# Kernel optimization log

Hardware: AMD Instinct MI355X
Metric: run time of the kernel (lower is better)

The kernel has to match this reference:

```python
import jax, jax.numpy as jnp
import numpy as np

N_NODES = 100000
N_EDGES = 1600000
NEG_SLOPE = 0.2


def gat_conv(x, W, al, ar, src, dst, n_nodes):
    """DGL-style GATConv. x:[N,Fin] W:[Fin,H*D] al,ar:[H,D] -> [N,H,D]."""
    H, D = al.shape
    h = (x @ W).reshape(-1, H, D)                      # [N,H,D]
    el = jnp.sum(h * al, axis=-1)                      # [N,H]
    er = jnp.sum(h * ar, axis=-1)                      # [N,H]
    e = jax.nn.leaky_relu(el[src] + er[dst], NEG_SLOPE)  # [E,H]
    # segment softmax over edges grouped by destination node
    m = jax.ops.segment_max(e, dst, num_segments=n_nodes)  # [N,H]
    ex = jnp.exp(e - m[dst])                           # [E,H]
    s = jax.ops.segment_sum(ex, dst, num_segments=n_nodes)  # [N,H]
    alpha = ex / s[dst]                                # [E,H]
    msg = h[src] * alpha[..., None]                    # [E,H,D]
    return jax.ops.segment_sum(msg, dst, num_segments=n_nodes)  # [N,H,D]


def setup_inputs() -> dict:
    key = jax.random.key(0)
    ks = jax.random.split(key, 9)
    in_dim, hid, out_dim, heads = 128, 32, 64, 4
    x = jax.random.normal(ks[0], (N_NODES, in_dim), dtype=jnp.float32)
    src = jax.random.randint(ks[1], (N_EDGES,), 0, N_NODES, dtype=jnp.int32)
    dst = jax.random.randint(ks[2], (N_EDGES,), 0, N_NODES, dtype=jnp.int32)
    sc1 = 1.0 / np.sqrt(in_dim)
    sc2 = 1.0 / np.sqrt(heads * hid)
    W1 = jax.random.normal(ks[3], (in_dim, heads * hid), dtype=jnp.float32) * sc1
    al1 = jax.random.normal(ks[4], (heads, hid), dtype=jnp.float32) * sc1
    ar1 = jax.random.normal(ks[5], (heads, hid), dtype=jnp.float32) * sc1
    W2 = jax.random.normal(ks[6], (heads * hid, out_dim), dtype=jnp.float32) * sc2
    al2 = jax.random.normal(ks[7], (1, out_dim), dtype=jnp.float32) * sc2
    ar2 = jax.random.normal(ks[8], (1, out_dim), dtype=jnp.float32) * sc2
    return {"x": x, "src": src, "dst": dst, "W1": W1, "al1": al1, "ar1": ar1,
            "W2": W2, "al2": al2, "ar2": ar2}


def reference(x, src, dst, W1, al1, ar1, W2, al2, ar2):
    h = gat_conv(x, W1, al1, ar1, src, dst, N_NODES)   # [N,4,32]
    h = h.reshape(h.shape[0], -1)                      # flatten(1) -> [N,128]
    h = jax.nn.selu(h)                                 # dropout is identity in eval
    out = gat_conv(h, W2, al2, ar2, src, dst, N_NODES) # [N,1,64]
    return out.mean(axis=1)                            # [N,64]
```

## Files before the change

kernel.cpp:

```cpp
#include <hip/hip_runtime.h>
#include <hip/hip_fp16.h>

#define N_NODES 100000
#define N_EDGES 1600000
#define NP1 (N_NODES + 1)
#define NB 391
#define CHUNK 6250
#define NBLK 256
#define BPAD 4736

typedef _Float16 half8 __attribute__((ext_vector_type(8)));
typedef float f32x4 __attribute__((ext_vector_type(4)));

static __device__ __forceinline__ unsigned pkh2(float a, float b) {
    __half2 t = __floats2half2_rn(a, b);
    return *(unsigned*)&t;
}

__global__ __launch_bounds__(256) void k_gemm1(
    const float* __restrict__ x, const float* __restrict__ W,
    const float* __restrict__ al, const float* __restrict__ ar,
    __half* __restrict__ h, float* __restrict__ el, float* __restrict__ er)
{
    __shared__ _Float16 Wt[128 * 136];
    __shared__ _Float16 xs[64 * 136];
    const int tid = threadIdx.x;
    const int n0 = blockIdx.x * 64;

    #pragma unroll
    for (int pass = 0; pass < 16; ++pass) {
        int k  = (tid >> 5) + pass * 8;
        int c4 = (tid & 31) * 4;
        float4 w = *(const float4*)(W + (size_t)k * 128 + c4);
        Wt[(c4 + 0) * 136 + k] = (_Float16)w.x;
        Wt[(c4 + 1) * 136 + k] = (_Float16)w.y;
        Wt[(c4 + 2) * 136 + k] = (_Float16)w.z;
        Wt[(c4 + 3) * 136 + k] = (_Float16)w.w;
    }
    {
        int row = tid >> 2, kq = (tid & 3) * 32;
        int n = n0 + row;
        _Float16* d = xs + row * 136 + kq;
        if (n < N_NODES) {
            const float* xp = x + (size_t)n * 128 + kq;
            #pragma unroll
            for (int j = 0; j < 8; ++j) {
                float4 v = *(const float4*)(xp + j * 4);
                d[j*4+0] = (_Float16)v.x; d[j*4+1] = (_Float16)v.y;
                d[j*4+2] = (_Float16)v.z; d[j*4+3] = (_Float16)v.w;
            }
        } else {
            #pragma unroll
            for (int j = 0; j < 32; ++j) d[j] = (_Float16)0.f;
        }
    }
    __syncthreads();

    const int wv = tid >> 6, l = tid & 63;
    const int r0 = wv * 16;
    const int lc = l & 15, lk = l >> 4;

    half8 afr[4];
    #pragma unroll
    for (int ks = 0; ks < 4; ++ks)
        afr[ks] = *(const half8*)(xs + (r0 + lc) * 136 + ks * 32 + lk * 8);
    __syncthreads();

    float eh_l[4][4], eh_r[4][4];
    #pragma unroll
    for (int hd = 0; hd < 4; ++hd)
        #pragma unroll
        for (int i = 0; i < 4; ++i) { eh_l[hd][i] = 0.f; eh_r[hd][i] = 0.f; }

    f32x4 accs[8];
    #pragma unroll
    for (int ct = 0; ct < 8; ++ct) {
        f32x4 acc = {0.f, 0.f, 0.f, 0.f};
        #pragma unroll
        for (int ks = 0; ks < 4; ++ks) {
            half8 b = *(const half8*)(Wt + (ct * 16 + lc) * 136 + ks * 32 + lk * 8);
            acc = __builtin_amdgcn_mfma_f32_16x16x32_f16(afr[ks], b, acc, 0, 0, 0);
        }
        accs[ct] = acc;
        float a_l = al[ct * 16 + lc], a_r = ar[ct * 16 + lc];
        #pragma unroll
        for (int i = 0; i < 4; ++i) {
            eh_l[ct >> 1][i] = fmaf(acc[i], a_l, eh_l[ct >> 1][i]);
            eh_r[ct >> 1][i] = fmaf(acc[i], a_r, eh_r[ct >> 1][i]);
        }
    }

    #pragma unroll
    for (int ct = 0; ct < 8; ++ct)
        #pragma unroll
        for (int i = 0; i < 4; ++i)
            xs[(r0 + lk * 4 + i) * 136 + ct * 16 + lc] = (_Float16)accs[ct][i];

    #pragma unroll
    for (int hd = 0; hd < 4; ++hd)
        #pragma unroll
        for (int i = 0; i < 4; ++i) {
            float v = eh_l[hd][i];
            v += __shfl_xor(v, 1); v += __shfl_xor(v, 2);
            v += __shfl_xor(v, 4); v += __shfl_xor(v, 8);
            eh_l[hd][i] = v;
            float u = eh_r[hd][i];
            u += __shfl_xor(u, 1); u += __shfl_xor(u, 2);
            u += __shfl_xor(u, 4); u += __shfl_xor(u, 8);
            eh_r[hd][i] = u;
        }
    if (lc == 0) {
        #pragma unroll
        for (int i = 0; i < 4; ++i) {
            int n = n0 + r0 + lk * 4 + i;
            if (n < N_NODES) {
                #pragma unroll
                for (int hd = 0; hd < 4; ++hd) {
                    el[n * 4 + hd] = eh_l[hd][i];
                    er[n * 4 + hd] = eh_r[hd][i];
                }
            }
        }
    }
    __syncthreads();
    {
        int row = tid >> 2, kq = (tid & 3) * 32;
        int n = n0 + row;
        if (n < N_NODES) {
            #pragma unroll
            for (int j = 0; j < 4; ++j)
                *(uint4*)(h + (size_t)n * 128 + kq + j * 8) =
                    *(const uint4*)(xs + row * 136 + kq + j * 8);
        }
    }
}

__global__ __launch_bounds__(256) void k_gemm2(
    const __half* __restrict__ in, const float* __restrict__ W,
    const float* __restrict__ al, const float* __restrict__ ar,
    __half* __restrict__ h, float* __restrict__ el, float* __restrict__ er)
{
    __shared__ _Float16 Wt[64 * 136];
    __shared__ _Float16 xs[64 * 136];
    const int tid = threadIdx.x;
    const int n0 = blockIdx.x * 64;
    const float SC = 1.0507009873554805f;
    const float AL = 1.6732632423543772f;

    #pragma unroll
    for (int pass = 0; pass < 8; ++pass) {
        int k  = (tid >> 4) + pass * 16;
        int c4 = (tid & 15) * 4;
        float4 w = *(const float4*)(W + (size_t)k * 64 + c4);
        Wt[(c4 + 0) * 136 + k] = (_Float16)w.x;
        Wt[(c4 + 1) * 136 + k] = (_Float16)w.y;
        Wt[(c4 + 2) * 136 + k] = (_Float16)w.z;
        Wt[(c4 + 3) * 136 + k] = (_Float16)w.w;
    }
    {
        int row = tid >> 2, kq = (tid & 3) * 32;
        int n = n0 + row;
        _Float16* d = xs + row * 136 + kq;
        if (n < N_NODES) {
            const __half* ip = in + (size_t)n * 128 + kq;
            #pragma unroll
            for (int j = 0; j < 8; ++j) {
                uint2 u = *(const uint2*)(ip + j * 4);
                float2 f01 = __half22float2(*(__half2*)&u.x);
                float2 f23 = __half22float2(*(__half2*)&u.y);
                float v0 = f01.x > 0.f ? SC * f01.x : SC * AL * (__expf(f01.x) - 1.f);
                float v1 = f01.y > 0.f ? SC * f01.y : SC * AL * (__expf(f01.y) - 1.f);
                float v2 = f23.x > 0.f ? SC * f23.x : SC * AL * (__expf(f23.x) - 1.f);
                float v3 = f23.y > 0.f ? SC * f23.y : SC * AL * (__expf(f23.y) - 1.f);
                d[j*4+0] = (_Float16)v0; d[j*4+1] = (_Float16)v1;
                d[j*4+2] = (_Float16)v2; d[j*4+3] = (_Float16)v3;
            }
        } else {
            #pragma unroll
            for (int j = 0; j < 32; ++j) d[j] = (_Float16)0.f;
        }
    }
    __syncthreads();

    const int wv = tid >> 6, l = tid & 63;
    const int r0 = wv * 16;
    const int lc = l & 15, lk = l >> 4;

    half8 afr[4];
    #pragma unroll
    for (int ks = 0; ks < 4; ++ks)
        afr[ks] = *(const half8*)(xs + (r0 + lc) * 136 + ks * 32 + lk * 8);
    __syncthreads();

    float pl[4], pr[4];
    #pragma unroll
    for (int i = 0; i < 4; ++i) { pl[i] = 0.f; pr[i] = 0.f; }

    f32x4 accs[4];
    #pragma unroll
    for (int ct = 0; ct < 4; ++ct) {
        f32x4 acc = {0.f, 0.f, 0.f, 0.f};
        #pragma unroll
        for (int ks = 0; ks < 4; ++ks) {
            half8 b = *(const half8*)(Wt + (ct * 16 + lc) * 136 + ks * 32 + lk * 8);
            acc = __builtin_amdgcn_mfma_f32_16x16x32_f16(afr[ks], b, acc, 0, 0, 0);
        }
        accs[ct] = acc;
        float a_l = al[ct * 16 + lc], a_r = ar[ct * 16 + lc];
        #pragma unroll
        for (int i = 0; i < 4; ++i) {
            pl[i] = fmaf(acc[i], a_l, pl[i]);
            pr[i] = fmaf(acc[i], a_r, pr[i]);
        }
    }

    #pragma unroll
    for (int ct = 0; ct < 4; ++ct)
        #pragma unroll
        for (int i = 0; i < 4; ++i)
            xs[(r0 + lk * 4 + i) * 136 + ct * 16 + lc] = (_Float16)accs[ct][i];

    #pragma unroll
    for (int i = 0; i < 4; ++i) {
        float v = pl[i];
        v += __shfl_xor(v, 1); v += __shfl_xor(v, 2);
        v += __shfl_xor(v, 4); v += __shfl_xor(v, 8);
        pl[i] = v;
        float u = pr[i];
        u += __shfl_xor(u, 1); u += __shfl_xor(u, 2);
        u += __shfl_xor(u, 4); u += __shfl_xor(u, 8);
        pr[i] = u;
    }
    if (lc == 0) {
        #pragma unroll
        for (int i = 0; i < 4; ++i) {
            int n = n0 + r0 + lk * 4 + i;
            if (n < N_NODES) { el[n] = pl[i]; er[n] = pr[i]; }
        }
    }
    __syncthreads();
    {
        int row = tid >> 2, kq = (tid & 3) * 16;
        int n = n0 + row;
        if (n < N_NODES) {
            #pragma unroll
            for (int j = 0; j < 2; ++j)
                *(uint4*)(h + (size_t)n * 64 + kq + j * 8) =
                    *(const uint4*)(xs + row * 136 + kq + j * 8);
        }
    }
}

__global__ __launch_bounds__(256) void k_place(
    const int* __restrict__ src, const int* __restrict__ dst,
    int* __restrict__ cursor, unsigned* __restrict__ pairs)
{
    __shared__ int cnt[NB], basev[NB];
    const int tid = threadIdx.x;
    for (int j = tid; j < NB; j += 256) cnt[j] = 0;
    __syncthreads();
    int beg = blockIdx.x * CHUNK, end = beg + CHUNK;
    for (int i = beg + tid; i < end; i += 256)
        atomicAdd(&cnt[dst[i] >> 8], 1);
    __syncthreads();
    for (int j = tid; j < NB; j += 256)
        basev[j] = cnt[j] ? atomicAdd(&cursor[j], cnt[j]) : 0;
    __syncthreads();
    for (int j = tid; j < NB; j += 256) cnt[j] = 0;
    __syncthreads();
    for (int i = beg + tid; i < end; i += 256) {
        int d = dst[i];
        int b = d >> 8;
        int r = atomicAdd(&cnt[b], 1);
        pairs[(size_t)b * BPAD + basev[b] + r] =
            ((unsigned)(d & 255) << 17) | (unsigned)src[i];
    }
}

__global__ __launch_bounds__(256) void k_csr(
    const unsigned* __restrict__ pairs, const int* __restrict__ cursor,
    unsigned* __restrict__ rowdeg, int* __restrict__ csr_src)
{
    __shared__ int cnt[256], exc[256];
    const int b = blockIdx.x;
    const int tid = threadIdx.x;
    cnt[tid] = 0;
    __syncthreads();
    int beg = b * BPAD;
    int end = beg + cursor[b];
    for (int i = beg + tid; i < end; i += 256)
        atomicAdd(&cnt[pairs[i] >> 17], 1);
    __syncthreads();
    int v = cnt[tid];
    exc[tid] = v;
    __syncthreads();
    for (int o = 1; o < 256; o <<= 1) {
        int t = (tid >= o) ? exc[tid - o] : 0;
        __syncthreads();
        exc[tid] += t;
        __syncthreads();
    }
    int excl = exc[tid] - v;
    int node = b * 256 + tid;
    if (node < N_NODES)
        rowdeg[node] = ((unsigned)(beg + excl) << 8) | (unsigned)v;
    __syncthreads();
    exc[tid] = beg + excl;
    cnt[tid] = 0;
    __syncthreads();
    for (int i = beg + tid; i < end; i += 256) {
        unsigned e = pairs[i];
        int dl = (int)(e >> 17);
        int r = atomicAdd(&cnt[dl], 1);
        csr_src[exc[dl] + r] = (int)(e & 0x1FFFFu);
    }
}

__global__ __launch_bounds__(256) void k_fused1(
    const unsigned* __restrict__ rowdeg, const int* __restrict__ csr_src,
    const __half* __restrict__ h,
    const float* __restrict__ el,
    const float* __restrict__ er,
    __half* __restrict__ out)
{
    __shared__ int    s_sx[4][64];
    __shared__ __half s_p[4][64][4];
    const int w = threadIdx.x >> 6;
    int node = (blockIdx.x << 2) + w;
    int lane = threadIdx.x & 63;
    if (node >= N_NODES) return;
    unsigned rd = rowdeg[node];
    int rs = (int)(rd >> 8), deg = (int)(rd & 255u);
    int re = rs + deg;
    const int q = lane & 15, g = lane >> 4;
    const int hq = q >> 2;
    float4 erd = ((const float4*)er)[node];
    float m0, m1, m2, m3;
    float s0 = 0.f, s1 = 0.f, s2 = 0.f, s3 = 0.f;
    __half2 acc2[4];
    #pragma unroll
    for (int k = 0; k < 4; ++k) acc2[k] = __half2half2((__half)0.f);

    auto agg = [&](int nch) {
        int nit4 = (nch + 15) >> 4;
        for (int t = 0; t < nit4; ++t) {
            int eb = t * 16 + g;
            int sj0 = s_sx[w][eb];
            int sj1 = s_sx[w][eb + 4];
            int sj2 = s_sx[w][eb + 8];
            int sj3 = s_sx[w][eb + 12];
            __half2 a0 = __half2half2(s_p[w][eb][hq]);
            __half2 a1 = __half2half2(s_p[w][eb + 4][hq]);
            __half2 a2 = __half2half2(s_p[w][eb + 8][hq]);
            __half2 a3 = __half2half2(s_p[w][eb + 12][hq]);
            uint4 v0 = *((const uint4*)(h + (size_t)sj0 * 128) + q);
            uint4 v1 = *((const uint4*)(h + (size_t)sj1 * 128) + q);
            uint4 v2 = *((const uint4*)(h + (size_t)sj2 * 128) + q);
            uint4 v3 = *((const uint4*)(h + (size_t)sj3 * 128) + q);
            acc2[0] = __hfma2(*(__half2*)&v0.x, a0, acc2[0]);
            acc2[1] = __hfma2(*(__half2*)&v0.y, a0, acc2[1]);
            acc2[2] = __hfma2(*(__half2*)&v0.z, a0, acc2[2]);
            acc2[3] = __hfma2(*(__half2*)&v0.w, a0, acc2[3]);
            acc2[0] = __hfma2(*(__half2*)&v1.x, a1, acc2[0]);
            acc2[1] = __hfma2(*(__half2*)&v1.y, a1, acc2[1]);
            acc2[2] = __hfma2(*(__half2*)&v1.z, a1, acc2[2]);
            acc2[3] = __hfma2(*(__half2*)&v1.w, a1, acc2[3]);
            acc2[0] = __hfma2(*(__half2*)&v2.x, a2, acc2[0]);
            acc2[1] = __hfma2(*(__half2*)&v2.y, a2, acc2[1]);
            acc2[2] = __hfma2(*(__half2*)&v2.z, a2, acc2[2]);
            acc2[3] = __hfma2(*(__half2*)&v2.w, a2, acc2[3]);
            acc2[0] = __hfma2(*(__half2*)&v3.x, a3, acc2[0]);
            acc2[1] = __hfma2(*(__half2*)&v3.y, a3, acc2[1]);
            acc2[2] = __hfma2(*(__half2*)&v3.z, a3, acc2[2]);
            acc2[3] = __hfma2(*(__half2*)&v3.w, a3, acc2[3]);
        }
    };

    if (re > rs) {
        int nch = min(64, re - rs);
        int sidx = 0;
        float e0 = -INFINITY, e1 = -INFINITY, e2 = -INFINITY, e3 = -INFINITY;
        if (lane < nch) {
            sidx = csr_src[rs + lane];
            float4 l4 = ((const float4*)el)[sidx];
            e0 = l4.x + erd.x; e0 = e0 >= 0.f ? e0 : 0.2f * e0;
            e1 = l4.y + erd.y; e1 = e1 >= 0.f ? e1 : 0.2f * e1;
            e2 = l4.z + erd.z; e2 = e2 >= 0.f ? e2 : 0.2f * e2;
            e3 = l4.w + erd.w; e3 = e3 >= 0.f ? e3 : 0.2f * e3;
        }
        float c0 = e0, c1 = e1, c2 = e2, c3 = e3;
        #pragma unroll
        for (int o = 32; o > 0; o >>= 1) {
            c0 = fmaxf(c0, __shfl_xor(c0, o));
            c1 = fmaxf(c1, __shfl_xor(c1, o));
            c2 = fmaxf(c2, __shfl_xor(c2, o));
            c3 = fmaxf(c3, __shfl_xor(c3, o));
        }
        m0 = c0; m1 = c1; m2 = c2; m3 = c3;
        float p0 = __expf(e0 - m0), p1 = __expf(e1 - m1);
        float p2 = __expf(e2 - m2), p3 = __expf(e3 - m3);
        s_sx[w][lane] = sidx;
        *(__half2*)&s_p[w][lane][0] = __floats2half2_rn(p0, p1);
        *(__half2*)&s_p[w][lane][2] = __floats2half2_rn(p2, p3);
        float q0 = p0, q1 = p1, q2 = p2, q3 = p3;
        #pragma unroll
        for (int o = 32; o > 0; o >>= 1) {
            q0 += __shfl_xor(q0, o);
            q1 += __shfl_xor(q1, o);
            q2 += __shfl_xor(q2, o);
            q3 += __shfl_xor(q3, o);
        }
        s0 = q0; s1 = q1; s2 = q2; s3 = q3;
        agg(nch);

        for (int base = rs + 64; base < re; base += 64) {
            nch = min(64, re - base);
            sidx = 0;
            e0 = e1 = e2 = e3 = -INFINITY;
            if (lane < nch) {
                sidx = csr_src[base + lane];
                float4 l4 = ((const float4*)el)[sidx];
                e0 = l4.x + erd.x; e0 = e0 >= 0.f ? e0 : 0.2f * e0;
                e1 = l4.y + erd.y; e1 = e1 >= 0.f ? e1 : 0.2f * e1;
                e2 = l4.z + erd.z; e2 = e2 >= 0.f ? e2 : 0.2f * e2;
                e3 = l4.w + erd.w; e3 = e3 >= 0.f ? e3 : 0.2f * e3;
            }
            c0 = e0; c1 = e1; c2 = e2; c3 = e3;
            #pragma unroll
            for (int o = 32; o > 0; o >>= 1) {
                c0 = fmaxf(c0, __shfl_xor(c0, o));
                c1 = fmaxf(c1, __shfl_xor(c1, o));
                c2 = fmaxf(c2, __shfl_xor(c2, o));
                c3 = fmaxf(c3, __shfl_xor(c3, o));
            }
            float n0 = fmaxf(m0, c0), n1 = fmaxf(m1, c1);
            float n2 = fmaxf(m2, c2), n3 = fmaxf(m3, c3);
            float r0 = __expf(m0 - n0), r1 = __expf(m1 - n1);
            float r2 = __expf(m2 - n2), r3 = __expf(m3 - n3);
            p0 = __expf(e0 - n0); p1 = __expf(e1 - n1);
            p2 = __expf(e2 - n2); p3 = __expf(e3 - n3);
            s_sx[w][lane] = sidx;
            *(__half2*)&s_p[w][lane][0] = __floats2half2_rn(p0, p1);
            *(__half2*)&s_p[w][lane][2] = __floats2half2_rn(p2, p3);
            q0 = p0; q1 = p1; q2 = p2; q3 = p3;
            #pragma unroll
            for (int o = 32; o > 0; o >>= 1) {
                q0 += __shfl_xor(q0, o);
                q1 += __shfl_xor(q1, o);
                q2 += __shfl_xor(q2, o);
                q3 += __shfl_xor(q3, o);
            }
            s0 = s0 * r0 + q0; s1 = s1 * r1 + q1;
            s2 = s2 * r2 + q2; s3 = s3 * r3 + q3;
            float rh = hq == 0 ? r0 : hq == 1 ? r1 : hq == 2 ? r2 : r3;
            __half2 rh2 = __half2half2((__half)rh);
            #pragma unroll
            for (int k = 0; k < 4; ++k) acc2[k] = __hmul2(acc2[k], rh2);
            m0 = n0; m1 = n1; m2 = n2; m3 = n3;
            agg(nch);
        }
    }

    float sh = hq == 0 ? s0 : hq == 1 ? s1 : hq == 2 ? s2 : s3;
    float inv = (re > rs) ? 1.f / sh : 0.f;
    float acc[8];
    #pragma unroll
    for (int k = 0; k < 4; ++k) {
        float2 f = __half22float2(acc2[k]);
        acc[2*k] = f.x * inv; acc[2*k+1] = f.y * inv;
    }
    #pragma unroll
    for (int k = 0; k < 8; ++k) {
        acc[k] += __shfl_xor(acc[k], 16);
        acc[k] += __shfl_xor(acc[k], 32);
    }
    if (g == 0) {
        uint4 o;
        o.x = pkh2(acc[0], acc[1]);
        o.y = pkh2(acc[2], acc[3]);
        o.z = pkh2(acc[4], acc[5]);
        o.w = pkh2(acc[6], acc[7]);
        *((uint4*)(out + (size_t)node * 128) + q) = o;
    }
}

__global__ __launch_bounds__(256) void k_fused2(
    const unsigned* __restrict__ rowdeg, const int* __restrict__ csr_src,
    const __half* __restrict__ h,
    const float* __restrict__ el,
    const float* __restrict__ er,
    float* __restrict__ out)
{
    __shared__ int    s_sx[4][64];
    __shared__ __half s_p[4][64];
    const int w = threadIdx.x >> 6;
    int node = (blockIdx.x << 2) + w;
    int lane = threadIdx.x & 63;
    if (node >= N_NODES) return;
    unsigned rd = rowdeg[node];
    int rs = (int)(rd >> 8), deg = (int)(rd & 255u);
    int re = rs + deg;
    const int q = lane & 7, g = lane >> 3;
    float erd = er[node];
    float m, s = 0.f;
    __half2 acc2[4];
    #pragma unroll
    for (int k = 0; k < 4; ++k) acc2[k] = __half2half2((__half)0.f);

    auto agg = [&](int nch) {
        int nit4 = (nch + 31) >> 5;
        for (int t = 0; t < nit4; ++t) {
            int eb = t * 32 + g;
            int sj0 = s_sx[w][eb];
            int sj1 = s_sx[w][eb + 8];
            int sj2 = s_sx[w][eb + 16];
            int sj3 = s_sx[w][eb + 24];
            __half2 a0 = __half2half2(s_p[w][eb]);
            __half2 a1 = __half2half2(s_p[w][eb + 8]);
            __half2 a2 = __half2half2(s_p[w][eb + 16]);
            __half2 a3 = __half2half2(s_p[w][eb + 24]);
            uint4 v0 = *((const uint4*)(h + (size_t)sj0 * 64) + q);
            uint4 v1 = *((const uint4*)(h + (size_t)sj1 * 64) + q);
            uint4 v2 = *((const uint4*)(h + (size_t)sj2 * 64) + q);
            uint4 v3 = *((const uint4*)(h + (size_t)sj3 * 64) + q);
            acc2[0] = __hfma2(*(__half2*)&v0.x, a0, acc2[0]);
            acc2[1] = __hfma2(*(__half2*)&v0.y, a0, acc2[1]);
            acc2[2] = __hfma2(*(__half2*)&v0.z, a0, acc2[2]);
            acc2[3] = __hfma2(*(__half2*)&v0.w, a0, acc2[3]);
            acc2[0] = __hfma2(*(__half2*)&v1.x, a1, acc2[0]);
            acc2[1] = __hfma2(*(__half2*)&v1.y, a1, acc2[1]);
            acc2[2] = __hfma2(*(__half2*)&v1.z, a1, acc2[2]);
            acc2[3] = __hfma2(*(__half2*)&v1.w, a1, acc2[3]);
            acc2[0] = __hfma2(*(__half2*)&v2.x, a2, acc2[0]);
            acc2[1] = __hfma2(*(__half2*)&v2.y, a2, acc2[1]);
            acc2[2] = __hfma2(*(__half2*)&v2.z, a2, acc2[2]);
            acc2[3] = __hfma2(*(__half2*)&v2.w, a2, acc2[3]);
            acc2[0] = __hfma2(*(__half2*)&v3.x, a3, acc2[0]);
            acc2[1] = __hfma2(*(__half2*)&v3.y, a3, acc2[1]);
            acc2[2] = __hfma2(*(__half2*)&v3.z, a3, acc2[2]);
            acc2[3] = __hfma2(*(__half2*)&v3.w, a3, acc2[3]);
        }
    };

    if (re > rs) {
        int nch = min(64, re - rs);
        int sidx = 0;
        float e = -INFINITY;
        if (lane < nch) {
            sidx = csr_src[rs + lane];
            e = el[sidx] + erd;
            e = e >= 0.f ? e : 0.2f * e;
        }
        float c = e;
        #pragma unroll
        for (int o = 32; o > 0; o >>= 1) c = fmaxf(c, __shfl_xor(c, o));
        m = c;
        float p = __expf(e - m);
        s_sx[w][lane] = sidx;
        s_p[w][lane] = (__half)p;
        float qq = p;
        #pragma unroll
        for (int o = 32; o > 0; o >>= 1) qq += __shfl_xor(qq, o);
        s = qq;
        agg(nch);

        for (int base = rs + 64; base < re; base += 64) {
            nch = min(64, re - base);
            sidx = 0;
            e = -INFINITY;
            if (lane < nch) {
                sidx = csr_src[base + lane];
                e = el[sidx] + erd;
                e = e >= 0.f ? e : 0.2f * e;
            }
            c = e;
            #pragma unroll
            for (int o = 32; o > 0; o >>= 1) c = fmaxf(c, __shfl_xor(c, o));
            float n = fmaxf(m, c);
            float r = __expf(m - n);
            p = __expf(e - n);
            s_sx[w][lane] = sidx;
            s_p[w][lane] = (__half)p;
            float qq2 = p;
            #pragma unroll
            for (int o = 32; o > 0; o >>= 1) qq2 += __shfl_xor(qq2, o);
            s = s * r + qq2;
            __half2 r2 = __half2half2((__half)r);
            #pragma unroll
            for (int k = 0; k < 4; ++k) acc2[k] = __hmul2(acc2[k], r2);
            m = n;
            agg(nch);
        }
    }

    float inv = (re > rs) ? 1.f / s : 0.f;
    float acc[8];
    #pragma unroll
    for (int k = 0; k < 4; ++k) {
        float2 f = __half22float2(acc2[k]);
        acc[2*k] = f.x * inv; acc[2*k+1] = f.y * inv;
    }
    #pragma unroll
    for (int k = 0; k < 8; ++k) {
        acc[k] += __shfl_xor(acc[k], 8);
        acc[k] += __shfl_xor(acc[k], 16);
        acc[k] += __shfl_xor(acc[k], 32);
    }
    if (g == 0) {
        float* op = out + (size_t)node * 64 + q * 8;
        *(float4*)(op)     = make_float4(acc[0], acc[1], acc[2], acc[3]);
        *(float4*)(op + 4) = make_float4(acc[4], acc[5], acc[6], acc[7]);
    }
}

extern "C" void kernel_launch(void* const* d_in, const int* in_sizes, int n_in,
                              void* d_out, int out_size, void* d_ws, size_t ws_size,
                              hipStream_t stream) {
    const float* x   = (const float*)d_in[0];
    const int*   src = (const int*)d_in[1];
    const int*   dst = (const int*)d_in[2];
    const float* W1  = (const float*)d_in[3];
    const float* al1 = (const float*)d_in[4];
    const float* ar1 = (const float*)d_in[5];
    const float* W2  = (const float*)d_in[6];
    const float* al2 = (const float*)d_in[7];
    const float* ar2 = (const float*)d_in[8];
    float* out = (float*)d_out;

    char* base = (char*)d_ws;
    __half* h1   = (__half*)base;   base += (size_t)N_NODES * 128 * 2;
    __half* out1 = (__half*)base;   base += (size_t)N_NODES * 128 * 2;
    float*  el1  = (float*)base;    base += (size_t)N_NODES * 4 * 4;
    float*  er1  = (float*)base;    base += (size_t)N_NODES * 4 * 4;
    unsigned* rowdeg = (unsigned*)base; base += (size_t)100004 * 4;
    int* cursor  = (int*)base;      base += 512 * 4;
    int* csr_src = (int*)base;      base += (size_t)NB * BPAD * 4;
    unsigned* pairs = (unsigned*)base; base += (size_t)NB * BPAD * 4;
    __half* h2   = h1;
    float*  el2  = (float*)((char*)h1 + (size_t)N_NODES * 64 * 2);
    float*  er2  = el2 + N_NODES;

    const int GB = (N_NODES + 63) / 64;

    hipMemsetAsync(cursor, 0, NB * sizeof(int), stream);
    k_place<<<NBLK, 256, 0, stream>>>(src, dst, cursor, pairs);
    k_csr<<<NB, 256, 0, stream>>>(pairs, cursor, rowdeg, csr_src);

    k_gemm1<<<GB, 256, 0, stream>>>(x, W1, al1, ar1, h1, el1, er1);
    k_fused1<<<(N_NODES + 3) / 4, 256, 0, stream>>>(rowdeg, csr_src, h1, el1, er1, out1);

    k_gemm2<<<GB, 256, 0, stream>>>(out1, W2, al2, ar2, h2, el2, er2);
    k_fused2<<<(N_NODES + 3) / 4, 256, 0, stream>>>(rowdeg, csr_src, h2, el2, er2, out);
}
```

Baseline: 237.2 us.

## Merge CSR build with GEMM1 and split layer-1 aggregation by head slices

Folds the CSR construction and the first GEMM into one launch, with block index selecting the role, so the two independent stages can run concurrently. The layer-1 hidden features are now stored head-major ([4][N][32]). The first aggregation kernel is restructured so each block handles one head for 8 nodes, which shrinks each gather to 64-byte rows and lets blocks for the same head share a smaller L2 working set. The cost is that the edge list, el values and softmax are reloaded and recomputed per head, about four times the index traffic. Cross-lane reductions are now done in half precision, which risks more rounding error.

```diff
diff --git a/kernel.cpp b/kernel.cpp
--- a/kernel.cpp
+++ b/kernel.cpp
@@ -3,11 +3,11 @@
 
 #define N_NODES 100000
 #define N_EDGES 1600000
-#define NP1 (N_NODES + 1)
 #define NB 391
 #define CHUNK 6250
 #define NBLK 256
 #define BPAD 4736
+#define GB1 1563
 
 typedef _Float16 half8 __attribute__((ext_vector_type(8)));
 typedef float f32x4 __attribute__((ext_vector_type(4)));
@@ -17,15 +17,21 @@
     return *(unsigned*)&t;
 }
 
-__global__ __launch_bounds__(256) void k_gemm1(
+static __device__ __forceinline__ __half2 shfl_xor_h2(__half2 v, int off) {
+    int t = __shfl_xor(*(int*)&v, off);
+    return *(__half2*)&t;
+}
+
+static __device__ void gemm1_body(
+    int blk, char* smem,
     const float* __restrict__ x, const float* __restrict__ W,
     const float* __restrict__ al, const float* __restrict__ ar,
-    __half* __restrict__ h, float* __restrict__ el, float* __restrict__ er)
+    _Float16* __restrict__ hs, float* __restrict__ el, float* __restrict__ er)
 {
-    __shared__ _Float16 Wt[128 * 136];
-    __shared__ _Float16 xs[64 * 136];
+    _Float16* Wt = (_Float16*)smem;
+    _Float16* xs = (_Float16*)(smem + 34816);
     const int tid = threadIdx.x;
-    const int n0 = blockIdx.x * 64;
+    const int n0 = blk * 64;
 
     #pragma unroll
     for (int pass = 0; pass < 16; ++pass) {
@@ -124,15 +130,70 @@
     }
     __syncthreads();
     {
-        int row = tid >> 2, kq = (tid & 3) * 32;
+        int row = tid >> 2, idx = tid & 3;
         int n = n0 + row;
         if (n < N_NODES) {
+            _Float16* dp = hs + ((size_t)idx * N_NODES + n) * 32;
+            const _Float16* sp = xs + row * 136 + idx * 32;
             #pragma unroll
             for (int j = 0; j < 4; ++j)
-                *(uint4*)(h + (size_t)n * 128 + kq + j * 8) =
-                    *(const uint4*)(xs + row * 136 + kq + j * 8);
-        }
-    }
+                *(uint4*)(dp + j * 8) = *(const uint4*)(sp + j * 8);
+        }
+    }
+}
+
+static __device__ void csr_body(
+    int b, char* smem,
+    const unsigned* __restrict__ pairs, const int* __restrict__ cursor,
+    unsigned* __restrict__ rowdeg, int* __restrict__ csr_src)
+{
+    int* cnt = (int*)smem;
+    int* exc = (int*)(smem + 1024);
+    const int tid = threadIdx.x;
+    cnt[tid] = 0;
+    __syncthreads();
+    int beg = b * BPAD;
+    int end = beg + cursor[b];
+    for (int i = beg + tid; i < end; i += 256)
+        atomicAdd(&cnt[pairs[i] >> 17], 1);
+    __syncthreads();
+    int v = cnt[tid];
+    exc[tid] = v;
+    __syncthreads();
+    for (int o = 1; o < 256; o <<= 1) {
+        int t = (tid >= o) ? exc[tid - o] : 0;
+        __syncthreads();
+        exc[tid] += t;
+        __syncthreads();
+    }
+    int excl = exc[tid] - v;
+    int node = b * 256 + tid;
+    if (node < N_NODES)
+        rowdeg[node] = ((unsigned)(beg + excl) << 8) | (unsigned)v;
+    __syncthreads();
+    exc[tid] = beg + excl;
+    cnt[tid] = 0;
+    __syncthreads();
+    for (int i = beg + tid; i < end; i += 256) {
+        unsigned e = pairs[i];
+        int dl = (int)(e >> 17);
+        int r = atomicAdd(&cnt[dl], 1);
+        csr_src[exc[dl] + r] = (int)(e & 0x1FFFFu);
+    }
+}
+
+__global__ __launch_bounds__(256) void k_mix1(
+    const float* __restrict__ x, const float* __restrict__ W,
+    const float* __restrict__ al, const float* __restrict__ ar,
+    _Float16* __restrict__ hs, float* __restrict__ el, float* __restrict__ er,
+    const unsigned* __restrict__ pairs, const int* __restrict__ cursor,
+    unsigned* __restrict__ rowdeg, int* __restrict__ csr_src)
+{
+    __shared__ __align__(16) char smem[52224];
+    if (blockIdx.x < NB)
+        csr_body(blockIdx.x, smem, pairs, cursor, rowdeg, csr_src);
+    else
+        gemm1_body(blockIdx.x - NB, smem, x, W, al, ar, hs, el, er);
 }
 
 __global__ __launch_bounds__(256) void k_gemm2(
@@ -277,210 +338,119 @@
     }
 }
 
-__global__ __launch_bounds__(256) void k_csr(
-    const unsigned* __restrict__ pairs, const int* __restrict__ cursor,
-    unsigned* __restrict__ rowdeg, int* __restrict__ csr_src)
-{
-    __shared__ int cnt[256], exc[256];
-    const int b = blockIdx.x;
-    const int tid = threadIdx.x;
-    cnt[tid] = 0;
-    __syncthreads();
-    int beg = b * BPAD;
-    int end = beg + cursor[b];
-    for (int i = beg + tid; i < end; i += 256)
-        atomicAdd(&cnt[pairs[i] >> 17], 1);
-    __syncthreads();
-    int v = cnt[tid];
-    exc[tid] = v;
-    __syncthreads();
-    for (int o = 1; o < 256; o <<= 1) {
-        int t = (tid >= o) ? exc[tid - o] : 0;
-        __syncthreads();
-        exc[tid] += t;
-        __syncthreads();
-    }
-    int excl = exc[tid] - v;
-    int node = b * 256 + tid;
-    if (node < N_NODES)
-        rowdeg[node] = ((unsigned)(beg + excl) << 8) | (unsigned)v;
-    __syncthreads();
-    exc[tid] = beg + excl;
-    cnt[tid] = 0;
-    __syncthreads();
-    for (int i = beg + tid; i < end; i += 256) {
-        unsigned e = pairs[i];
-        int dl = (int)(e >> 17);
-        int r = atomicAdd(&cnt[dl], 1);
-        csr_src[exc[dl] + r] = (int)(e & 0x1FFFFu);
-    }
-}
-
 __global__ __launch_bounds__(256) void k_fused1(
     const unsigned* __restrict__ rowdeg, const int* __restrict__ csr_src,
-    const __half* __restrict__ h,
+    const _Float16* __restrict__ hs,
     const float* __restrict__ el,
     const float* __restrict__ er,
     __half* __restrict__ out)
 {
     __shared__ int    s_sx[4][64];
-    __shared__ __half s_p[4][64][4];
+    __shared__ __half s_ph[4][64];
     const int w = threadIdx.x >> 6;
-    int node = (blockIdx.x << 2) + w;
-    int lane = threadIdx.x & 63;
-    if (node >= N_NODES) return;
-    unsigned rd = rowdeg[node];
-    int rs = (int)(rd >> 8), deg = (int)(rd & 255u);
-    int re = rs + deg;
-    const int q = lane & 15, g = lane >> 4;
-    const int hq = q >> 2;
-    float4 erd = ((const float4*)er)[node];
-    float m0, m1, m2, m3;
-    float s0 = 0.f, s1 = 0.f, s2 = 0.f, s3 = 0.f;
-    __half2 acc2[4];
-    #pragma unroll
-    for (int k = 0; k < 4; ++k) acc2[k] = __half2half2((__half)0.f);
-
-    auto agg = [&](int nch) {
-        int nit4 = (nch + 15) >> 4;
-        for (int t = 0; t < nit4; ++t) {
-            int eb = t * 16 + g;
-            int sj0 = s_sx[w][eb];
-            int sj1 = s_sx[w][eb + 4];
-            int sj2 = s_sx[w][eb + 8];
-            int sj3 = s_sx[w][eb + 12];
-            __half2 a0 = __half2half2(s_p[w][eb][hq]);
-            __half2 a1 = __half2half2(s_p[w][eb + 4][hq]);
-            __half2 a2 = __half2half2(s_p[w][eb + 8][hq]);
-            __half2 a3 = __half2half2(s_p[w][eb + 12][hq]);
-            uint4 v0 = *((const uint4*)(h + (size_t)sj0 * 128) + q);
-            uint4 v1 = *((const uint4*)(h + (size_t)sj1 * 128) + q);
-            uint4 v2 = *((const uint4*)(h + (size_t)sj2 * 128) + q);
-            uint4 v3 = *((const uint4*)(h + (size_t)sj3 * 128) + q);
-            acc2[0] = __hfma2(*(__half2*)&v0.x, a0, acc2[0]);
-            acc2[1] = __hfma2(*(__half2*)&v0.y, a0, acc2[1]);
-            acc2[2] = __hfma2(*(__half2*)&v0.z, a0, acc2[2]);
-            acc2[3] = __hfma2(*(__half2*)&v0.w, a0, acc2[3]);
-            acc2[0] = __hfma2(*(__half2*)&v1.x, a1, acc2[0]);
-            acc2[1] = __hfma2(*(__half2*)&v1.y, a1, acc2[1]);
-            acc2[2] = __hfma2(*(__half2*)&v1.z, a1, acc2[2]);
-            acc2[3] = __hfma2(*(__half2*)&v1.w, a1, acc2[3]);
-            acc2[0] = __hfma2(*(__half2*)&v2.x, a2, acc2[0]);
-            acc2[1] = __hfma2(*(__half2*)&v2.y, a2, acc2[1]);
-            acc2[2] = __hfma2(*(__half2*)&v2.z, a2, acc2[2]);
-            acc2[3] = __hfma2(*(__half2*)&v2.w, a2, acc2[3]);
-            acc2[0] = __hfma2(*(__half2*)&v3.x, a3, acc2[0]);
-            acc2[1] = __hfma2(*(__half2*)&v3.y, a3, acc2[1]);
-            acc2[2] = __hfma2(*(__half2*)&v3.z, a3, acc2[2]);
-            acc2[3] = __hfma2(*(__half2*)&v3.w, a3, acc2[3]);
-        }
-    };
-
-    if (re > rs) {
-        int nch = min(64, re - rs);
-        int sidx = 0;
-        float e0 = -INFINITY, e1 = -INFINITY, e2 = -INFINITY, e3 = -INFINITY;
-        if (lane < nch) {
-            sidx = csr_src[rs + lane];
-            float4 l4 = ((const float4*)el)[sidx];
-            e0 = l4.x + erd.x; e0 = e0 >= 0.f ? e0 : 0.2f * e0;
-            e1 = l4.y + erd.y; e1 = e1 >= 0.f ? e1 : 0.2f * e1;
-            e2 = l4.z + erd.z; e2 = e2 >= 0.f ? e2 : 0.2f * e2;
-            e3 = l4.w + erd.w; e3 = e3 >= 0.f ? e3 : 0.2f * e3;
-        }
-        float c0 = e0, c1 = e1, c2 = e2, c3 = e3;
-        #pragma unroll
-        for (int o = 32; o > 0; o >>= 1) {
-            c0 = fmaxf(c0, __shfl_xor(c0, o));
-            c1 = fmaxf(c1, __shfl_xor(c1, o));
-            c2 = fmaxf(c2, __shfl_xor(c2, o));
-            c3 = fmaxf(c3, __shfl_xor(c3, o));
-        }
-        m0 = c0; m1 = c1; m2 = c2; m3 = c3;
-        float p0 = __expf(e0 - m0), p1 = __expf(e1 - m1);
-        float p2 = __expf(e2 - m2), p3 = __expf(e3 - m3);
-        s_sx[w][lane] = sidx;
-        *(__half2*)&s_p[w][lane][0] = __floats2half2_rn(p0, p1);
-        *(__half2*)&s_p[w][lane][2] = __floats2half2_rn(p2, p3);
-        float q0 = p0, q1 = p1, q2 = p2, q3 = p3;
-        #pragma unroll
-        for (int o = 32; o > 0; o >>= 1) {
-            q0 += __shfl_xor(q0, o);
-            q1 += __shfl_xor(q1, o);
-            q2 += __shfl_xor(q2, o);
-            q3 += __shfl_xor(q3, o);
-        }
-        s0 = q0; s1 = q1; s2 = q2; s3 = q3;
-        agg(nch);
-
-        for (int base = rs + 64; base < re; base += 64) {
-            nch = min(64, re - base);
-            sidx = 0;
-            e0 = e1 = e2 = e3 = -INFINITY;
+    const int lane = threadIdx.x & 63;
+    const int s = blockIdx.x & 3;
+    const int c = blockIdx.x >> 2;
+    const int q = lane & 3, g = lane >> 2;
+    const _Float16* hbase = hs + (size_t)s * N_NODES * 32;
+
+    #pragma unroll 1
+    for (int ni = 0; ni < 2; ++ni) {
+        int nd = c * 8 + w * 2 + ni;
+        unsigned rd = rowdeg[nd];
+        int rs = (int)(rd >> 8), deg = (int)(rd & 255u);
+        int re = rs + deg;
+        float erd = er[nd * 4 + s];
+        float m, ssum = 0.f;
+        __half2 acc2[4];
+        #pragma unroll
+        for (int k = 0; k < 4; ++k) acc2[k] = __half2half2((__half)0.f);
+
+        auto agg = [&](int nch) {
+            int nit = (nch + 15) >> 4;
+            for (int t = 0; t < nit; ++t) {
+                int eb = t * 16 + g;
+                int sj = s_sx[w][eb];
+                __half2 a = __half2half2(s_ph[w][eb]);
+                uint4 v = *((const uint4*)(hbase + (size_t)sj * 32) + q);
+                acc2[0] = __hfma2(*(__half2*)&v.x, a, acc2[0]);
+                acc2[1] = __hfma2(*(__half2*)&v.y, a, acc2[1]);
+                acc2[2] = __hfma2(*(__half2*)&v.z, a, acc2[2]);
+                acc2[3] = __hfma2(*(__half2*)&v.w, a, acc2[3]);
+            }
+        };
+
+        if (deg > 0) {
+            int nch = min(64, deg);
+            int sidx = 0;
+            float e = -INFINITY;
             if (lane < nch) {
-                sidx = csr_src[base + lane];
-                float4 l4 = ((const float4*)el)[sidx];
-                e0 = l4.x + erd.x; e0 = e0 >= 0.f ? e0 : 0.2f * e0;
-                e1 = l4.y + erd.y; e1 = e1 >= 0.f ? e1 : 0.2f * e1;
-                e2 = l4.z + erd.z; e2 = e2 >= 0.f ? e2 : 0.2f * e2;
-                e3 = l4.w + erd.w; e3 = e3 >= 0.f ? e3 : 0.2f * e3;
+                sidx = csr_src[rs + lane];
+                e = el[sidx * 4 + s] + erd;
+                e = e >= 0.f ? e : 0.2f * e;
             }
-            c0 = e0; c1 = e1; c2 = e2; c3 = e3;
-            #pragma unroll
-            for (int o = 32; o > 0; o >>= 1) {
-                c0 = fmaxf(c0, __shfl_xor(c0, o));
-                c1 = fmaxf(c1, __shfl_xor(c1, o));
-                c2 = fmaxf(c2, __shfl_xor(c2, o));
-                c3 = fmaxf(c3, __shfl_xor(c3, o));
+            float cmx = e;
+            #pragma unroll
+            for (int o = 32; o > 0; o >>= 1) cmx = fmaxf(cmx, __shfl_xor(cmx, o));
+            m = cmx;
+            float p = __expf(e - m);
+            s_sx[w][lane] = sidx;
+            s_ph[w][lane] = (__half)p;
+            float qq = p;
+            #pragma unroll
+            for (int o = 32; o > 0; o >>= 1) qq += __shfl_xor(qq, o);
+            ssum = qq;
+            agg(nch);
+
+            for (int base = rs + 64; base < re; base += 64) {
+                nch = min(64, re - base);
+                sidx = 0;
+                e = -INFINITY;
+                if (lane < nch) {
+                    sidx = csr_src[base + lane];
+                    e = el[sidx * 4 + s] + erd;
+                    e = e >= 0.f ? e : 0.2f * e;
+                }
+                cmx = e;
+                #pragma unroll
+                for (int o = 32; o > 0; o >>= 1) cmx = fmaxf(cmx, __shfl_xor(cmx, o));
+                float n = fmaxf(m, cmx);
+                float r = __expf(m - n);
+                p = __expf(e - n);
+                s_sx[w][lane] = sidx;
+                s_ph[w][lane] = (__half)p;
+                float qq2 = p;
+                #pragma unroll
+                for (int o = 32; o > 0; o >>= 1) qq2 += __shfl_xor(qq2, o);
+                ssum = ssum * r + qq2;
+                __half2 r2 = __half2half2((__half)r);
+                #pragma unroll
+                for (int k = 0; k < 4; ++k) acc2[k] = __hmul2(acc2[k], r2);
+                m = n;
+                agg(nch);
             }
-            float n0 = fmaxf(m0, c0), n1 = fmaxf(m1, c1);
-            float n2 = fmaxf(m2, c2), n3 = fmaxf(m3, c3);
-            float r0 = __expf(m0 - n0), r1 = __expf(m1 - n1);
-            float r2 = __expf(m2 - n2), r3 = __expf(m3 - n3);
-            p0 = __expf(e0 - n0); p1 = __expf(e1 - n1);
-            p2 = __expf(e2 - n2); p3 = __expf(e3 - n3);
-            s_sx[w][lane] = sidx;
-            *(__half2*)&s_p[w][lane][0] = __floats2half2_rn(p0, p1);
-            *(__half2*)&s_p[w][lane][2] = __floats2half2_rn(p2, p3);
-            q0 = p0; q1 = p1; q2 = p2; q3 = p3;
-            #pragma unroll
-            for (int o = 32; o > 0; o >>= 1) {
-                q0 += __shfl_xor(q0, o);
-                q1 += __shfl_xor(q1, o);
-                q2 += __shfl_xor(q2, o);
-                q3 += __shfl_xor(q3, o);
-            }
-            s0 = s0 * r0 + q0; s1 = s1 * r1 + q1;
-            s2 = s2 * r2 + q2; s3 = s3 * r3 + q3;
-            float rh = hq == 0 ? r0 : hq == 1 ? r1 : hq == 2 ? r2 : r3;
-            __half2 rh2 = __half2half2((__half)rh);
-            #pragma unroll
-            for (int k = 0; k < 4; ++k) acc2[k] = __hmul2(acc2[k], rh2);
-            m0 = n0; m1 = n1; m2 = n2; m3 = n3;
-            agg(nch);
-        }
-    }
-
-    float sh = hq == 0 ? s0 : hq == 1 ? s1 : hq == 2 ? s2 : s3;
-    float inv = (re > rs) ? 1.f / sh : 0.f;
-    float acc[8];
-    #pragma unroll
-    for (int k = 0; k < 4; ++k) {
-        float2 f = __half22float2(acc2[k]);
-        acc[2*k] = f.x * inv; acc[2*k+1] = f.y * inv;
-    }
-    #pragma unroll
-    for (int k = 0; k < 8; ++k) {
-        acc[k] += __shfl_xor(acc[k], 16);
-        acc[k] += __shfl_xor(acc[k], 32);
-    }
-    if (g == 0) {
-        uint4 o;
-        o.x = pkh2(acc[0], acc[1]);
-        o.y = pkh2(acc[2], acc[3]);
-        o.z = pkh2(acc[4], acc[5]);
-        o.w = pkh2(acc[6], acc[7]);
-        *((uint4*)(out + (size_t)node * 128) + q) = o;
+        }
+
+        #pragma unroll
+        for (int k = 0; k < 4; ++k) {
+            acc2[k] = __hadd2(acc2[k], shfl_xor_h2(acc2[k], 4));
+            acc2[k] = __hadd2(acc2[k], shfl_xor_h2(acc2[k], 8));
+            acc2[k] = __hadd2(acc2[k], shfl_xor_h2(acc2[k], 16));
+            acc2[k] = __hadd2(acc2[k], shfl_xor_h2(acc2[k], 32));
+        }
+        if (g == 0) {
+            float inv = (deg > 0) ? 1.f / ssum : 0.f;
+            float2 f0 = __half22float2(acc2[0]);
+            float2 f1 = __half22float2(acc2[1]);
+            float2 f2 = __half22float2(acc2[2]);
+            float2 f3 = __half22float2(acc2[3]);
+            uint4 o;
+            o.x = pkh2(f0.x * inv, f0.y * inv);
+            o.y = pkh2(f1.x * inv, f1.y * inv);
+            o.z = pkh2(f2.x * inv, f2.y * inv);
+            o.w = pkh2(f3.x * inv, f3.y * inv);
+            *(uint4*)(out + (size_t)nd * 128 + s * 32 + q * 8) = o;
+        }
     }
 }
 
@@ -628,27 +598,27 @@
     float* out = (float*)d_out;
 
     char* base = (char*)d_ws;
-    __half* h1   = (__half*)base;   base += (size_t)N_NODES * 128 * 2;
-    __half* out1 = (__half*)base;   base += (size_t)N_NODES * 128 * 2;
+    _Float16* h1s  = (_Float16*)base; base += (size_t)N_NODES * 128 * 2;
+    __half*   out1 = (__half*)base;   base += (size_t)N_NODES * 128 * 2;
     float*  el1  = (float*)base;    base += (size_t)N_NODES * 4 * 4;
     float*  er1  = (float*)base;    base += (size_t)N_NODES * 4 * 4;
     unsigned* rowdeg = (unsigned*)base; base += (size_t)100004 * 4;
     int* cursor  = (int*)base;      base += 512 * 4;
     int* csr_src = (int*)base;      base += (size_t)NB * BPAD * 4;
     unsigned* pairs = (unsigned*)base; base += (size_t)NB * BPAD * 4;
-    __half* h2   = h1;
-    float*  el2  = (float*)((char*)h1 + (size_t)N_NODES * 64 * 2);
+    __half* h2   = (__half*)h1s;
+    float*  el2  = (float*)((char*)h1s + (size_t)N_NODES * 64 * 2);
     float*  er2  = el2 + N_NODES;
-
-    const int GB = (N_NODES + 63) / 64;
 
     hipMemsetAsync(cursor, 0, NB * sizeof(int), stream);
     k_place<<<NBLK, 256, 0, stream>>>(src, dst, cursor, pairs);
-    k_csr<<<NB, 256, 0, stream>>>(pairs, cursor, rowdeg, csr_src);
-
-    k_gemm1<<<GB, 256, 0, stream>>>(x, W1, al1, ar1, h1, el1, er1);
-    k_fused1<<<(N_NODES + 3) / 4, 256, 0, stream>>>(rowdeg, csr_src, h1, el1, er1, out1);
-
-    k_gemm2<<<GB, 256, 0, stream>>>(out1, W2, al2, ar2, h2, el2, er2);
+
+    k_mix1<<<NB + GB1, 256, 0, stream>>>(x, W1, al1, ar1, h1s, el1, er1,
+                                         pairs, cursor, rowdeg, csr_src);
+
+    k_fused1<<<(N_NODES / 8) * 4, 256, 0, stream>>>(rowdeg, csr_src, h1s,
+                                                    el1, er1, out1);
+
+    k_gemm2<<<(N_NODES + 63) / 64, 256, 0, stream>>>(out1, W2, al2, ar2, h2, el2, er2);
     k_fused2<<<(N_NODES + 3) / 4, 256, 0, stream>>>(rowdeg, csr_src, h2, el2, er2, out);
 }
```

Result: slower. 295.8 us (+24.7%).
